# Kernel tuning notes

Measured on AMD Instinct MI355X. Metric: run time of the kernel, lower is better.

## Reference

```python
import jax, jax.numpy as jnp
import numpy as np

B, Q, S, D, H = 4, 1024, 4096, 256, 8
HD = D // H
NEG = -1000000000.0


def setup_inputs() -> dict:
    key = jax.random.key(0)
    ks = jax.random.split(key, 12)
    s = 1.0 / np.sqrt(D)
    inp = {
        "query": jax.random.normal(ks[0], (B, Q, D), jnp.float32),
        "key": jax.random.normal(ks[1], (B, S, D), jnp.float32),
        "value": jax.random.normal(ks[2], (B, S, D), jnp.float32),
        "attention_mask": jax.random.randint(ks[3], (B, Q, S), 0, 2) > 0,
        # nn.Linear weights stored as [out, in]; we apply x @ W.T + b
        "wq": jax.random.uniform(ks[4], (D, D), jnp.float32, -s, s),
        "bq": jnp.zeros((D,), jnp.float32),
        "wk": jax.random.uniform(ks[5], (D, D), jnp.float32, -s, s),
        "bk": jnp.zeros((D,), jnp.float32),
        "wv": jax.random.uniform(ks[6], (D, D), jnp.float32, -s, s),
        "bv": jnp.zeros((D,), jnp.float32),
        "wo": jax.random.uniform(ks[7], (D, D), jnp.float32, -s, s),
        "bo": jnp.zeros((D,), jnp.float32),
        "ln_g": jnp.ones((D,), jnp.float32),
        "ln_b": jnp.zeros((D,), jnp.float32),
    }
    return inp


def _layernorm(x, g, b, eps=1e-5):
    mu = jnp.mean(x, axis=-1, keepdims=True)
    var = jnp.var(x, axis=-1, keepdims=True)
    return (x - mu) * jax.lax.rsqrt(var + eps) * g + b


def reference(query, key, value, attention_mask, wq, bq, wk, bk, wv, bv, wo, bo, ln_g, ln_b):
    residual = query
    x = _layernorm(query, ln_g, ln_b)
    q = x @ wq.T + bq                       # [B,Q,D]
    k = key @ wk.T + bk                     # [B,S,D]
    v = value @ wv.T + bv                   # [B,S,D]
    q = q.reshape(B, Q, H, HD).transpose(0, 2, 1, 3)   # [B,H,Q,HD]
    k = k.reshape(B, S, H, HD).transpose(0, 2, 1, 3)   # [B,H,S,HD]
    v = v.reshape(B, S, H, HD).transpose(0, 2, 1, 3)   # [B,H,S,HD]
    scale = HD ** -0.5
    scores = jnp.einsum("bhqd,bhsd->bhqs", q, k) * scale   # [B,H,Q,S]
    scores = jnp.where(attention_mask[:, None, :, :], scores, NEG)
    attn = jax.nn.softmax(scores, axis=-1)
    # dropout is identity in eval/inference mode
    out = jnp.einsum("bhqs,bhsd->bhqd", attn, v)            # [B,H,Q,HD]
    out = out.transpose(0, 2, 1, 3).reshape(B, Q, D)
    out = out @ wo.T + bo
    return out + residual
```

## Files before the change

### kernel.cpp

```cpp
#include <hip/hip_runtime.h>
#include <cmath>

#define BQ 4
#define QL 1024
#define SL 4096
#define DM 256
#define NH 8
#define HD 32
#define NROWS 32768
#define NSPLIT 4
#define SEG (SL / NSPLIT)

typedef __attribute__((ext_vector_type(8))) short short8;
typedef __attribute__((ext_vector_type(4))) short short4v;
typedef __attribute__((ext_vector_type(4))) float f32x4;
typedef __attribute__((ext_vector_type(4))) unsigned int uint4v;
typedef unsigned long long u64;

#define MFMA16(a, b, c) __builtin_amdgcn_mfma_f32_16x16x32_bf16((a), (b), (c), 0, 0, 0)

__device__ __forceinline__ short f2bf(float f) {
  union { float f; unsigned int u; } x; x.f = f;
  unsigned int r = x.u + 0x7FFFu + ((x.u >> 16) & 1u);
  return (short)(r >> 16);
}
__device__ __forceinline__ unsigned int fu(float f) {
  union { float f; unsigned int u; } x; x.f = f; return x.u;
}

#define CVT_CHUNKS 1081344
__global__ __launch_bounds__(256) void cvt_kernel(const float* __restrict__ key,
                                                  const float* __restrict__ value,
                                                  const float* __restrict__ wq,
                                                  const float* __restrict__ wk,
                                                  const float* __restrict__ wv,
                                                  const float* __restrict__ wo,
                                                  const uint4v* __restrict__ mask4,
                                                  unsigned int* __restrict__ flags,
                                                  short* __restrict__ kb16,
                                                  short* __restrict__ vb16,
                                                  short* __restrict__ w16) {
  if (blockIdx.x == 0) {
    __shared__ int fA, fB;
    if (threadIdx.x == 0) { fA = 0; fB = 0; }
    __syncthreads();
    unsigned int a = 0, bb = 0;
#pragma unroll
    for (int i = 0; i < 16; ++i) {
      uint4v v = mask4[threadIdx.x * 16 + i];
#pragma unroll
      for (int e = 0; e < 4; ++e) {
        a |= (v[e] & 0xFEFEFEFEu);
        bb |= (v[e] & 0xFFFFFF00u);
      }
    }
    if (a) atomicOr(&fA, 1);
    if (bb) atomicOr(&fB, 1);
    __syncthreads();
    if (threadIdx.x == 0) flags[0] = (fA || !fB) ? 4u : 1u;
  }
  for (int i = blockIdx.x * 256 + threadIdx.x; i < CVT_CHUNKS; i += gridDim.x * 256) {
    const float* src;
    short* dst;
    if (i < 524288) {
      src = key + (size_t)i * 8; dst = kb16 + (size_t)i * 8;
    } else if (i < 1048576) {
      const int j = i - 524288;
      src = value + (size_t)j * 8; dst = vb16 + (size_t)j * 8;
    } else {
      int j = i - 1048576;
      if (j < 8192)       { src = wq + j * 8;            dst = w16 + j * 8; }
      else if (j < 16384) { src = wk + (j - 8192) * 8;   dst = w16 + 65536 + (j - 8192) * 8; }
      else if (j < 24576) { src = wv + (j - 16384) * 8;  dst = w16 + 131072 + (j - 16384) * 8; }
      else                { src = wo + (j - 24576) * 8;  dst = w16 + 196608 + (j - 24576) * 8; }
    }
    f32x4 a0 = *(const f32x4*)src;
    f32x4 a1 = *(const f32x4*)(src + 4);
    short8 o;
#pragma unroll
    for (int e = 0; e < 4; ++e) { o[e] = f2bf(a0[e]); o[4 + e] = f2bf(a1[e]); }
    *(short8*)dst = o;
  }
}

__global__ __launch_bounds__(256) void maskbits_kernel(const void* __restrict__ mask,
                                                       const unsigned int* __restrict__ flags,
                                                       u64* __restrict__ MB) {
  const int i = blockIdx.x * 256 + threadIdx.x;
  u64 bits = 0;
  if (flags[0] == 4u) {
    const uint4v* src = (const uint4v*)mask + (size_t)i * 16;
#pragma unroll
    for (int c = 0; c < 16; ++c) {
      uint4v v = src[c];
      unsigned int nib = 0;
#pragma unroll
      for (int e = 0; e < 4; ++e) nib |= (v[e] != 0u ? 1u : 0u) << e;
      bits |= (u64)nib << ((c & 3) * 16 + (c >> 2) * 4);
    }
  } else {
    const uint4v* src = (const uint4v*)mask + (size_t)i * 4;
#pragma unroll
    for (int c = 0; c < 4; ++c) {
      uint4v v = src[c];
#pragma unroll
      for (int e4 = 0; e4 < 4; ++e4) {
        const unsigned int u = v[e4];
        unsigned int nib = 0;
        nib |= (u & 0x000000FFu) ? 1u : 0u;
        nib |= (u & 0x0000FF00u) ? 2u : 0u;
        nib |= (u & 0x00FF0000u) ? 4u : 0u;
        nib |= (u & 0xFF000000u) ? 8u : 0u;
        bits |= (u64)nib << (e4 * 16 + c * 4);
      }
    }
  }
  MB[i] = bits;
}

__global__ __launch_bounds__(256) void ln_q_kernel(const float* __restrict__ x,
                                                   const float* __restrict__ gw,
                                                   const float* __restrict__ bw,
                                                   short* __restrict__ out) {
  const int lane = threadIdx.x & 63;
  const int row = blockIdx.x * 4 + (threadIdx.x >> 6);
  const float* xr = x + (size_t)row * DM;
  f32x4 v = *(const f32x4*)(xr + lane * 4);
  float s = v[0] + v[1] + v[2] + v[3];
  float s2 = v[0]*v[0] + v[1]*v[1] + v[2]*v[2] + v[3]*v[3];
#pragma unroll
  for (int m = 1; m < 64; m <<= 1) { s += __shfl_xor(s, m); s2 += __shfl_xor(s2, m); }
  const float mu = s * (1.0f / DM);
  const float var = s2 * (1.0f / DM) - mu * mu;
  const float inv = rsqrtf(var + 1e-5f);
  f32x4 gv = *(const f32x4*)(gw + lane * 4);
  f32x4 bv = *(const f32x4*)(bw + lane * 4);
  short4v o;
#pragma unroll
  for (int i = 0; i < 4; ++i) o[i] = f2bf((v[i] - mu) * inv * gv[i] + bv[i]);
  *(short4v*)(out + (size_t)row * DM + lane * 4) = o;
}

template <int EPI>
__global__ __launch_bounds__(256) void gemm_bt(const short* __restrict__ A,
                                               const short* __restrict__ W16,
                                               const float* __restrict__ bias,
                                               void* __restrict__ outp,
                                               const float* __restrict__ resid,
                                               float oscale) {
  __shared__ __align__(16) short As[64][72];
  __shared__ __align__(16) short Bs[64][72];
  const int t = threadIdx.x;
  const int lane = t & 63, w = t >> 6;
  const int wm = w >> 1, wn = w & 1;
  const int g = lane >> 4, lr = lane & 15, gsh = g * 4;
  const int bid = blockIdx.x;
  const int x = bid & 7, j = bid >> 3;
  const int mt8 = gridDim.x >> 5;
  const int m0 = (x * mt8 + (j >> 2)) * 64;
  const int n0 = (j & 3) * 64;
  const int row = (t * 2) >> 3, cc0 = (t * 2) & 7;
  f32x4 acc[2][2] = {};

  short8 an[2], bn[2];
#pragma unroll
  for (int c = 0; c < 2; ++c) {
    an[c] = *(const short8*)(A + (size_t)(m0 + row) * DM + (cc0 + c) * 8);
    bn[c] = *(const short8*)(W16 + (size_t)(n0 + row) * DM + (cc0 + c) * 8);
  }
  for (int k0 = 0; k0 < DM; k0 += 64) {
    if (k0) __syncthreads();
#pragma unroll
    for (int c = 0; c < 2; ++c) {
      *(short8*)&As[row][(cc0 + c) * 8] = an[c];
      *(short8*)&Bs[row][(cc0 + c) * 8] = bn[c];
    }
    __syncthreads();
    if (k0 < DM - 64) {
#pragma unroll
      for (int c = 0; c < 2; ++c) {
        an[c] = *(const short8*)(A + (size_t)(m0 + row) * DM + k0 + 64 + (cc0 + c) * 8);
        bn[c] = *(const short8*)(W16 + (size_t)(n0 + row) * DM + k0 + 64 + (cc0 + c) * 8);
      }
    }
#pragma unroll
    for (int ks = 0; ks < 2; ++ks) {
      short8 af[2], bfr[2];
#pragma unroll
      for (int i = 0; i < 2; ++i) af[i] = *(const short8*)&As[wm * 32 + i * 16 + lr][ks * 32 + g * 8];
#pragma unroll
      for (int jj = 0; jj < 2; ++jj) bfr[jj] = *(const short8*)&Bs[wn * 32 + jj * 16 + lr][ks * 32 + g * 8];
#pragma unroll
      for (int i = 0; i < 2; ++i)
#pragma unroll
        for (int jj = 0; jj < 2; ++jj) acc[i][jj] = MFMA16(af[i], bfr[jj], acc[i][jj]);
    }
  }
  if (EPI == 2) {
#pragma unroll
    for (int i = 0; i < 2; ++i)
#pragma unroll
      for (int jj = 0; jj < 2; ++jj)
#pragma unroll
        for (int r = 0; r < 4; ++r) {
          const int rr = m0 + wm * 32 + i * 16 + gsh + r;
          const int col = n0 + wn * 32 + jj * 16 + lr;
          ((float*)outp)[(size_t)rr * DM + col] =
              acc[i][jj][r] + bias[col] + resid[(size_t)rr * DM + col];
        }
  } else if (EPI == 0 || EPI == 1) {
    __syncthreads();
#pragma unroll
    for (int i = 0; i < 2; ++i)
#pragma unroll
      for (int jj = 0; jj < 2; ++jj) {
        const int nl = wn * 32 + jj * 16 + lr;
        const float bv = bias[n0 + nl];
#pragma unroll
        for (int r = 0; r < 4; ++r)
          As[wm * 32 + i * 16 + gsh + r][nl] = f2bf((acc[i][jj][r] + bv) * oscale);
      }
    __syncthreads();
#pragma unroll
    for (int c = 0; c < 2; ++c) {
      const int idx = t * 2 + c, dl = idx >> 3, ch = idx & 7;
      *(short8*)((short*)outp + (size_t)(m0 + dl) * DM + n0 + ch * 8) =
          *(const short8*)&As[dl][ch * 8];
    }
  } else {
    __syncthreads();
#pragma unroll
    for (int i = 0; i < 2; ++i)
#pragma unroll
      for (int jj = 0; jj < 2; ++jj) {
        const int nl = wn * 32 + jj * 16 + lr;
        const float bv = bias[n0 + nl];
        short4v pk4;
#pragma unroll
        for (int r = 0; r < 4; ++r) pk4[r] = f2bf(acc[i][jj][r] + bv);
        *(short4v*)&As[nl][wm * 32 + i * 16 + gsh] = pk4;
      }
    __syncthreads();
    const int bidx = m0 >> 12, sbase = m0 & (SL - 1);
#pragma unroll
    for (int c = 0; c < 2; ++c) {
      const int idx = t * 2 + c, dl = idx >> 3, ch = idx & 7;
      *(short8*)((short*)outp + ((size_t)bidx * DM + n0 + dl) * SL + sbase + ch * 8) =
          *(const short8*)&As[dl][ch * 8];
    }
  }
}

__global__ __launch_bounds__(256, 4) void attn_kernel(const short* __restrict__ qb,
                                                      const short* __restrict__ kb,
                                                      const short* __restrict__ vbT,
                                                      const unsigned short* __restrict__ MB,
                                                      float* __restrict__ Op,
                                                      float* __restrict__ Lp) {
  __shared__ __align__(16) short Ks[2][64][40];
  __shared__ __align__(16) short Vs[2][32][76];

  const int n_ = blockIdx.x;
  const int x_ = n_ & 7, j_ = n_ >> 3;
  const int grp = ((j_ >> 5) << 3) + x_;
  const int within = j_ & 31;
  const int q0 = (within & 7) * 128;
  const int quarter = within >> 3;
  const int h = grp & 7, b = grp >> 3;

  const int t = threadIdx.x;
  const int l = t & 63, w = t >> 6;
  const int g = l >> 4, lr = l & 15, gsh = g * 4;
  const int qbase = q0 + w * 32;
  const int srow = t >> 2, scc = t & 3;
  const int vd = t >> 3, vsc = t & 7;

  const short* Kp = kb + ((size_t)b * SL + quarter * SEG + srow) * DM + h * HD + scc * 8;
  const short* Vp = vbT + ((size_t)(b * NH + h) * HD + vd) * SL + quarter * SEG + vsc * 8;
  const unsigned short* MBp0 =
      MB + (((size_t)(b * QL) + qbase + lr) * 64 + quarter * (SEG / 64)) * 4 + g;
  const unsigned short* MBp1 = MBp0 + 16 * 64 * 4;

  const short8 qf0 =
      *(const short8*)(qb + ((size_t)(b * QL) + qbase + lr) * DM + h * HD + g * 8);
  const short8 qf1 =
      *(const short8*)(qb + ((size_t)(b * QL) + qbase + 16 + lr) * DM + h * HD + g * 8);

  const short ONE = (short)0x3F80;
  const short8 ONES = {ONE, ONE, ONE, ONE, ONE, ONE, ONE, ONE};
  f32x4 Ov0[2] = {}, Ov1[2] = {};
  f32x4 Ls0 = {0.f, 0.f, 0.f, 0.f}, Ls1 = {0.f, 0.f, 0.f, 0.f};

  short8 kreg = *(const short8*)Kp;
  short8 vreg = *(const short8*)Vp;
  unsigned int mb0 = MBp0[0], mb1 = MBp1[0];

#pragma unroll 2
  for (int it = 0; it < SEG / 64; ++it) {
    const int buf = it & 1;
    *(short8*)&Ks[buf][srow][scc * 8] = kreg;
    {
      short4v lo = {vreg[0], vreg[1], vreg[2], vreg[3]};
      short4v hi = {vreg[4], vreg[5], vreg[6], vreg[7]};
      *(short4v*)&Vs[buf][vd][vsc * 8] = lo;
      *(short4v*)&Vs[buf][vd][vsc * 8 + 4] = hi;
    }
    __syncthreads();
    if (it < SEG / 64 - 1) {
      kreg = *(const short8*)(Kp + (size_t)(it + 1) * 64 * DM);
      vreg = *(const short8*)(Vp + (it + 1) * 64);
      mb0 = MBp0[(it + 1) * 4];
      mb1 = MBp1[(it + 1) * 4];
    }

    const f32x4 z = {0.f, 0.f, 0.f, 0.f};
    f32x4 sc0[4], sc1[4];
#pragma unroll
    for (int f = 0; f < 4; ++f) {
      short8 kf = *(const short8*)&Ks[buf][f * 16 + lr][g * 8];
      sc0[f] = MFMA16(kf, qf0, z);
      sc1[f] = MFMA16(kf, qf1, z);
    }
#pragma unroll
    for (int ks = 0; ks < 2; ++ks) {
      unsigned int pk0[2][2], pk1[2][2];
#pragma unroll
      for (int fi = 0; fi < 2; ++fi) {
        const int f = 2 * ks + fi;
        unsigned int p0[4], p1[4];
#pragma unroll
        for (int r = 0; r < 4; ++r) {
          const unsigned int m0b = (unsigned int)(-(int)((mb0 >> (f * 4 + r)) & 1u));
          const unsigned int m1b = (unsigned int)(-(int)((mb1 >> (f * 4 + r)) & 1u));
          p0[r] = fu(__builtin_amdgcn_exp2f(sc0[f][r])) & m0b;
          p1[r] = fu(__builtin_amdgcn_exp2f(sc1[f][r])) & m1b;
        }
        pk0[fi][0] = __builtin_amdgcn_perm(p0[0], p0[1], 0x03020706u);
        pk0[fi][1] = __builtin_amdgcn_perm(p0[2], p0[3], 0x03020706u);
        pk1[fi][0] = __builtin_amdgcn_perm(p1[0], p1[1], 0x03020706u);
        pk1[fi][1] = __builtin_amdgcn_perm(p1[2], p1[3], 0x03020706u);
      }
      union { unsigned int u[4]; short8 v; } pa0, pa1;
      pa0.u[0] = pk0[0][0]; pa0.u[1] = pk0[0][1]; pa0.u[2] = pk0[1][0]; pa0.u[3] = pk0[1][1];
      pa1.u[0] = pk1[0][0]; pa1.u[1] = pk1[0][1]; pa1.u[2] = pk1[1][0]; pa1.u[3] = pk1[1][1];
      Ls0 = MFMA16(pa0.v, ONES, Ls0);
      Ls1 = MFMA16(pa1.v, ONES, Ls1);
#pragma unroll
      for (int n = 0; n < 2; ++n) {
        short4v va = *(const short4v*)&Vs[buf][n * 16 + lr][(2 * ks) * 16 + gsh];
        short4v vb2 = *(const short4v*)&Vs[buf][n * 16 + lr][(2 * ks + 1) * 16 + gsh];
        union { short4v h[2]; short8 v; } vf;
        vf.h[0] = va; vf.h[1] = vb2;
        Ov0[n] = MFMA16(pa0.v, vf.v, Ov0[n]);
        Ov1[n] = MFMA16(pa1.v, vf.v, Ov1[n]);
      }
    }
  }
  const int ridx = (b * NH + h) * QL + qbase;
  const size_t pb = (size_t)quarter * NROWS + ridx;
#pragma unroll
  for (int n = 0; n < 2; ++n)
#pragma unroll
    for (int r = 0; r < 4; ++r) {
      Op[(pb + gsh + r) * 32 + n * 16 + lr] = Ov0[n][r];
      Op[(pb + 16 + gsh + r) * 32 + n * 16 + lr] = Ov1[n][r];
    }
  if (lr == 0) {
#pragma unroll
    for (int r = 0; r < 4; ++r) {
      Lp[pb + gsh + r] = Ls0[r];
      Lp[pb + 16 + gsh + r] = Ls1[r];
    }
  }
}

__global__ __launch_bounds__(256) void combine_kernel(const float* __restrict__ Op,
                                                      const float* __restrict__ Lp,
                                                      short* __restrict__ ao) {
  const int tid = blockIdx.x * 256 + threadIdx.x;
  const int r = tid >> 3;
  const int dq = (tid & 7) * 4;
  float den = 0.0f;
  f32x4 acc = {0.f, 0.f, 0.f, 0.f};
#pragma unroll
  for (int i = 0; i < NSPLIT; ++i) {
    den += Lp[(size_t)i * NROWS + r];
    const f32x4 o = *(const f32x4*)(Op + ((size_t)i * NROWS + r) * 32 + dq);
#pragma unroll
    for (int e = 0; e < 4; ++e) acc[e] += o[e];
  }
  const float inv = __builtin_amdgcn_rcpf(den);
  const int b = r >> 13, h = (r >> 10) & 7, q = r & 1023;
  short4v o;
#pragma unroll
  for (int i = 0; i < 4; ++i) o[i] = f2bf(acc[i] * inv);
  *(short4v*)(ao + ((size_t)(b * QL + q)) * DM + h * HD + dq) = o;
}

extern "C" void kernel_launch(void* const* d_in, const int* in_sizes, int n_in,
                              void* d_out, int out_size, void* d_ws, size_t ws_size,
                              hipStream_t stream) {
  const float* query = (const float*)d_in[0];
  const float* key   = (const float*)d_in[1];
  const float* value = (const float*)d_in[2];
  const void*  mask  = d_in[3];
  const float* wq = (const float*)d_in[4];
  const float* bq = (const float*)d_in[5];
  const float* wk = (const float*)d_in[6];
  const float* bk = (const float*)d_in[7];
  const float* wv = (const float*)d_in[8];
  const float* bv = (const float*)d_in[9];
  const float* wo = (const float*)d_in[10];
  const float* bo = (const float*)d_in[11];
  const float* lng = (const float*)d_in[12];
  const float* lnb = (const float*)d_in[13];
  float* out = (float*)d_out;

  char* ws = (char*)d_ws;
  unsigned int* flags = (unsigned int*)ws;
  float* Lp  = (float*)(ws + (4u << 10));
  short* xln = (short*)(ws + (2u << 20));
  short* qb  = (short*)(ws + (4u << 20));
  short* kb  = (short*)(ws + (6u << 20));
  short* vbT = (short*)(ws + (14u << 20));
  u64*   mbt = (u64*)(ws + (22u << 20));
  short* w16 = (short*)(ws + (24u << 20));
  char*  pool = ws + (25u << 20);
  short* kb16 = (short*)pool;
  short* vb16 = (short*)(pool + (8u << 20));
  float* Op = (float*)pool;
  short* ao = (short*)(pool + (16u << 20));

  const float qscale = (float)(1.4426950408889634 / sqrt((double)HD));

  cvt_kernel<<<2048, 256, 0, stream>>>(key, value, wq, wk, wv, wo,
                                       (const uint4v*)mask, flags, kb16, vb16, w16);
  maskbits_kernel<<<1024, 256, 0, stream>>>(mask, flags, mbt);
  ln_q_kernel<<<(BQ * QL) / 4, 256, 0, stream>>>(query, lng, lnb, xln);
  gemm_bt<0><<<(BQ * QL / 64) * 4, 256, 0, stream>>>(xln, w16, bq, qb, nullptr, qscale);
  gemm_bt<1><<<(BQ * SL / 64) * 4, 256, 0, stream>>>(kb16, w16 + 65536, bk, kb, nullptr, 1.0f);
  gemm_bt<3><<<(BQ * SL / 64) * 4, 256, 0, stream>>>(vb16, w16 + 131072, bv, vbT, nullptr, 1.0f);
  attn_kernel<<<1024, 256, 0, stream>>>(qb, kb, vbT, (const unsigned short*)mbt, Op, Lp);
  combine_kernel<<<1024, 256, 0, stream>>>(Op, Lp, ao);
  gemm_bt<2><<<(BQ * QL / 64) * 4, 256, 0, stream>>>(ao, w16 + 196608, bo, out, query, 1.0f);
}
```

Baseline: 95.12 us.

## Fuse fp32-to-bf16 conversion into K/V GEMMs, double attention split, bf16 partials

```diff
diff --git a/kernel.cpp b/kernel.cpp
--- a/kernel.cpp
+++ b/kernel.cpp
@@ -8,7 +8,7 @@
 #define NH 8
 #define HD 32
 #define NROWS 32768
-#define NSPLIT 4
+#define NSPLIT 8
 #define SEG (SL / NSPLIT)
 
 typedef __attribute__((ext_vector_type(8))) short short8;
@@ -27,19 +27,19 @@
 __device__ __forceinline__ unsigned int fu(float f) {
   union { float f; unsigned int u; } x; x.f = f; return x.u;
 }
-
-#define CVT_CHUNKS 1081344
-__global__ __launch_bounds__(256) void cvt_kernel(const float* __restrict__ key,
-                                                  const float* __restrict__ value,
-                                                  const float* __restrict__ wq,
-                                                  const float* __restrict__ wk,
-                                                  const float* __restrict__ wv,
-                                                  const float* __restrict__ wo,
-                                                  const uint4v* __restrict__ mask4,
-                                                  unsigned int* __restrict__ flags,
-                                                  short* __restrict__ kb16,
-                                                  short* __restrict__ vb16,
-                                                  short* __restrict__ w16) {
+__device__ __forceinline__ float bf2f(short s) {
+  union { float f; unsigned int u; } x;
+  x.u = ((unsigned int)(unsigned short)s) << 16;
+  return x.f;
+}
+
+__global__ __launch_bounds__(256) void wcvt_kernel(const float* __restrict__ wq,
+                                                   const float* __restrict__ wk,
+                                                   const float* __restrict__ wv,
+                                                   const float* __restrict__ wo,
+                                                   const uint4v* __restrict__ mask4,
+                                                   unsigned int* __restrict__ flags,
+                                                   short* __restrict__ w16) {
   if (blockIdx.x == 0) {
     __shared__ int fA, fB;
     if (threadIdx.x == 0) { fA = 0; fB = 0; }
@@ -59,28 +59,19 @@
     __syncthreads();
     if (threadIdx.x == 0) flags[0] = (fA || !fB) ? 4u : 1u;
   }
-  for (int i = blockIdx.x * 256 + threadIdx.x; i < CVT_CHUNKS; i += gridDim.x * 256) {
-    const float* src;
-    short* dst;
-    if (i < 524288) {
-      src = key + (size_t)i * 8; dst = kb16 + (size_t)i * 8;
-    } else if (i < 1048576) {
-      const int j = i - 524288;
-      src = value + (size_t)j * 8; dst = vb16 + (size_t)j * 8;
-    } else {
-      int j = i - 1048576;
-      if (j < 8192)       { src = wq + j * 8;            dst = w16 + j * 8; }
-      else if (j < 16384) { src = wk + (j - 8192) * 8;   dst = w16 + 65536 + (j - 8192) * 8; }
-      else if (j < 24576) { src = wv + (j - 16384) * 8;  dst = w16 + 131072 + (j - 16384) * 8; }
-      else                { src = wo + (j - 24576) * 8;  dst = w16 + 196608 + (j - 24576) * 8; }
-    }
-    f32x4 a0 = *(const f32x4*)src;
-    f32x4 a1 = *(const f32x4*)(src + 4);
-    short8 o;
-#pragma unroll
-    for (int e = 0; e < 4; ++e) { o[e] = f2bf(a0[e]); o[4 + e] = f2bf(a1[e]); }
-    *(short8*)dst = o;
-  }
+  const int i = blockIdx.x * 256 + threadIdx.x;
+  const float* src;
+  short* dst;
+  if (i < 8192)       { src = wq + i * 8;            dst = w16 + i * 8; }
+  else if (i < 16384) { src = wk + (i - 8192) * 8;   dst = w16 + 65536 + (i - 8192) * 8; }
+  else if (i < 24576) { src = wv + (i - 16384) * 8;  dst = w16 + 131072 + (i - 16384) * 8; }
+  else                { src = wo + (i - 24576) * 8;  dst = w16 + 196608 + (i - 24576) * 8; }
+  f32x4 a0 = *(const f32x4*)src;
+  f32x4 a1 = *(const f32x4*)(src + 4);
+  short8 o;
+#pragma unroll
+  for (int e = 0; e < 4; ++e) { o[e] = f2bf(a0[e]); o[4 + e] = f2bf(a1[e]); }
+  *(short8*)dst = o;
 }
 
 __global__ __launch_bounds__(256) void maskbits_kernel(const void* __restrict__ mask,
@@ -141,8 +132,8 @@
   *(short4v*)(out + (size_t)row * DM + lane * 4) = o;
 }
 
-template <int EPI>
-__global__ __launch_bounds__(256) void gemm_bt(const short* __restrict__ A,
+template <int AF32, int EPI>
+__global__ __launch_bounds__(256) void gemm_bt(const void* __restrict__ Ap,
                                                const short* __restrict__ W16,
                                                const float* __restrict__ bias,
                                                void* __restrict__ outp,
@@ -162,24 +153,47 @@
   const int row = (t * 2) >> 3, cc0 = (t * 2) & 7;
   f32x4 acc[2][2] = {};
 
-  short8 an[2], bn[2];
+  const float* Af = (const float*)Ap;
+  const short* A16 = (const short*)Ap;
+  f32x4 apf[2][2];
+  short8 aps[2];
+  short8 bn[2];
 #pragma unroll
   for (int c = 0; c < 2; ++c) {
-    an[c] = *(const short8*)(A + (size_t)(m0 + row) * DM + (cc0 + c) * 8);
+    if (AF32) {
+      const float* s = Af + (size_t)(m0 + row) * DM + (cc0 + c) * 8;
+      apf[c][0] = *(const f32x4*)s;
+      apf[c][1] = *(const f32x4*)(s + 4);
+    } else {
+      aps[c] = *(const short8*)(A16 + (size_t)(m0 + row) * DM + (cc0 + c) * 8);
+    }
     bn[c] = *(const short8*)(W16 + (size_t)(n0 + row) * DM + (cc0 + c) * 8);
   }
   for (int k0 = 0; k0 < DM; k0 += 64) {
     if (k0) __syncthreads();
 #pragma unroll
     for (int c = 0; c < 2; ++c) {
-      *(short8*)&As[row][(cc0 + c) * 8] = an[c];
+      short8 sv;
+      if (AF32) {
+#pragma unroll
+        for (int e = 0; e < 4; ++e) { sv[e] = f2bf(apf[c][0][e]); sv[4 + e] = f2bf(apf[c][1][e]); }
+      } else {
+        sv = aps[c];
+      }
+      *(short8*)&As[row][(cc0 + c) * 8] = sv;
       *(short8*)&Bs[row][(cc0 + c) * 8] = bn[c];
     }
     __syncthreads();
     if (k0 < DM - 64) {
 #pragma unroll
       for (int c = 0; c < 2; ++c) {
-        an[c] = *(const short8*)(A + (size_t)(m0 + row) * DM + k0 + 64 + (cc0 + c) * 8);
+        if (AF32) {
+          const float* s = Af + (size_t)(m0 + row) * DM + k0 + 64 + (cc0 + c) * 8;
+          apf[c][0] = *(const f32x4*)s;
+          apf[c][1] = *(const f32x4*)(s + 4);
+        } else {
+          aps[c] = *(const short8*)(A16 + (size_t)(m0 + row) * DM + k0 + 64 + (cc0 + c) * 8);
+        }
         bn[c] = *(const short8*)(W16 + (size_t)(n0 + row) * DM + k0 + 64 + (cc0 + c) * 8);
       }
     }
@@ -251,21 +265,21 @@
   }
 }
 
-__global__ __launch_bounds__(256, 4) void attn_kernel(const short* __restrict__ qb,
+__global__ __launch_bounds__(256, 8) void attn_kernel(const short* __restrict__ qb,
                                                       const short* __restrict__ kb,
                                                       const short* __restrict__ vbT,
                                                       const unsigned short* __restrict__ MB,
-                                                      float* __restrict__ Op,
+                                                      short* __restrict__ Op,
                                                       float* __restrict__ Lp) {
   __shared__ __align__(16) short Ks[2][64][40];
   __shared__ __align__(16) short Vs[2][32][76];
 
   const int n_ = blockIdx.x;
   const int x_ = n_ & 7, j_ = n_ >> 3;
-  const int grp = ((j_ >> 5) << 3) + x_;
-  const int within = j_ & 31;
+  const int grp = ((j_ >> 6) << 3) + x_;
+  const int within = j_ & 63;
   const int q0 = (within & 7) * 128;
-  const int quarter = within >> 3;
+  const int split = within >> 3;
   const int h = grp & 7, b = grp >> 3;
 
   const int t = threadIdx.x;
@@ -275,10 +289,10 @@
   const int srow = t >> 2, scc = t & 3;
   const int vd = t >> 3, vsc = t & 7;
 
-  const short* Kp = kb + ((size_t)b * SL + quarter * SEG + srow) * DM + h * HD + scc * 8;
-  const short* Vp = vbT + ((size_t)(b * NH + h) * HD + vd) * SL + quarter * SEG + vsc * 8;
+  const short* Kp = kb + ((size_t)b * SL + split * SEG + srow) * DM + h * HD + scc * 8;
+  const short* Vp = vbT + ((size_t)(b * NH + h) * HD + vd) * SL + split * SEG + vsc * 8;
   const unsigned short* MBp0 =
-      MB + (((size_t)(b * QL) + qbase + lr) * 64 + quarter * (SEG / 64)) * 4 + g;
+      MB + (((size_t)(b * QL) + qbase + lr) * 64 + split * (SEG / 64)) * 4 + g;
   const unsigned short* MBp1 = MBp0 + 16 * 64 * 4;
 
   const short8 qf0 =
@@ -357,13 +371,13 @@
     }
   }
   const int ridx = (b * NH + h) * QL + qbase;
-  const size_t pb = (size_t)quarter * NROWS + ridx;
+  const size_t pb = (size_t)split * NROWS + ridx;
 #pragma unroll
   for (int n = 0; n < 2; ++n)
 #pragma unroll
     for (int r = 0; r < 4; ++r) {
-      Op[(pb + gsh + r) * 32 + n * 16 + lr] = Ov0[n][r];
-      Op[(pb + 16 + gsh + r) * 32 + n * 16 + lr] = Ov1[n][r];
+      Op[(pb + gsh + r) * 32 + n * 16 + lr] = f2bf(Ov0[n][r]);
+      Op[(pb + 16 + gsh + r) * 32 + n * 16 + lr] = f2bf(Ov1[n][r]);
     }
   if (lr == 0) {
 #pragma unroll
@@ -374,7 +388,7 @@
   }
 }
 
-__global__ __launch_bounds__(256) void combine_kernel(const float* __restrict__ Op,
+__global__ __launch_bounds__(256) void combine_kernel(const short* __restrict__ Op,
                                                       const float* __restrict__ Lp,
                                                       short* __restrict__ ao) {
   const int tid = blockIdx.x * 256 + threadIdx.x;
@@ -385,9 +399,9 @@
 #pragma unroll
   for (int i = 0; i < NSPLIT; ++i) {
     den += Lp[(size_t)i * NROWS + r];
-    const f32x4 o = *(const f32x4*)(Op + ((size_t)i * NROWS + r) * 32 + dq);
-#pragma unroll
-    for (int e = 0; e < 4; ++e) acc[e] += o[e];
+    const short4v o = *(const short4v*)(Op + ((size_t)i * NROWS + r) * 32 + dq);
+#pragma unroll
+    for (int e = 0; e < 4; ++e) acc[e] += bf2f(o[e]);
   }
   const float inv = __builtin_amdgcn_rcpf(den);
   const int b = r >> 13, h = (r >> 10) & 7, q = r & 1023;
@@ -425,22 +439,18 @@
   short* vbT = (short*)(ws + (14u << 20));
   u64*   mbt = (u64*)(ws + (22u << 20));
   short* w16 = (short*)(ws + (24u << 20));
-  char*  pool = ws + (25u << 20);
-  short* kb16 = (short*)pool;
-  short* vb16 = (short*)(pool + (8u << 20));
-  float* Op = (float*)pool;
-  short* ao = (short*)(pool + (16u << 20));
+  short* Op  = (short*)(ws + (25u << 20));
+  short* ao  = (short*)(ws + (41u << 20));
 
   const float qscale = (float)(1.4426950408889634 / sqrt((double)HD));
 
-  cvt_kernel<<<2048, 256, 0, stream>>>(key, value, wq, wk, wv, wo,
-                                       (const uint4v*)mask, flags, kb16, vb16, w16);
+  wcvt_kernel<<<128, 256, 0, stream>>>(wq, wk, wv, wo, (const uint4v*)mask, flags, w16);
   maskbits_kernel<<<1024, 256, 0, stream>>>(mask, flags, mbt);
   ln_q_kernel<<<(BQ * QL) / 4, 256, 0, stream>>>(query, lng, lnb, xln);
-  gemm_bt<0><<<(BQ * QL / 64) * 4, 256, 0, stream>>>(xln, w16, bq, qb, nullptr, qscale);
-  gemm_bt<1><<<(BQ * SL / 64) * 4, 256, 0, stream>>>(kb16, w16 + 65536, bk, kb, nullptr, 1.0f);
-  gemm_bt<3><<<(BQ * SL / 64) * 4, 256, 0, stream>>>(vb16, w16 + 131072, bv, vbT, nullptr, 1.0f);
-  attn_kernel<<<1024, 256, 0, stream>>>(qb, kb, vbT, (const unsigned short*)mbt, Op, Lp);
+  gemm_bt<0, 0><<<(BQ * QL / 64) * 4, 256, 0, stream>>>(xln, w16, bq, qb, nullptr, qscale);
+  gemm_bt<1, 1><<<(BQ * SL / 64) * 4, 256, 0, stream>>>(key, w16 + 65536, bk, kb, nullptr, 1.0f);
+  gemm_bt<1, 3><<<(BQ * SL / 64) * 4, 256, 0, stream>>>(value, w16 + 131072, bv, vbT, nullptr, 1.0f);
+  attn_kernel<<<2048, 256, 0, stream>>>(qb, kb, vbT, (const unsigned short*)mbt, Op, Lp);
   combine_kernel<<<1024, 256, 0, stream>>>(Op, Lp, ao);
-  gemm_bt<2><<<(BQ * QL / 64) * 4, 256, 0, stream>>>(ao, w16 + 196608, bo, out, query, 1.0f);
-}
+  gemm_bt<0, 2><<<(BQ * QL / 64) * 4, 256, 0, stream>>>(ao, w16 + 196608, bo, out, query, 1.0f);
+}
```

Result: slower. 162.4 us (+70.8%).
